# Optimization experiments

Hardware: AMD Instinct MI355X
Metric: run time of the kernel (lower is better)

The kernel has to match this reference:

```python
import jax, jax.numpy as jnp
import numpy as np

B, S = 2, 1024
ENC_IN, MARK_IN = 21, 4
PRED_LEN, C_OUT = 96, 21
E = 512                 # embedding_dim
INNER = 2 * E           # proj_factor=2.0 (library default; Model does not pass it)
NH = 8                  # mLSTM heads
DH = INNER // NH        # 128
K = 4                   # causal conv1d kernel
BS = 4                  # qkv_proj_blocksize
NHP = INNER // BS       # 256 block-diagonal proj heads
NB = 4                  # num_blocks
EPS = 1e-5


def setup_inputs() -> dict:
    key = jax.random.key(0)
    ks = jax.random.split(key, 24)
    it = iter(range(24))
    def n(shape, s=0.02):
        return jax.random.normal(ks[next(it)], shape, jnp.float32) * s
    return {
        "x_enc": n((B, S, ENC_IN), 1.0),
        "x_mark_enc": n((B, S, MARK_IN), 1.0),
        "x_dec": n((B, PRED_LEN, ENC_IN), 1.0),
        "x_mark_dec": n((B, PRED_LEN, MARK_IN), 1.0),
        "emb_W": n((ENC_IN + MARK_IN, E), 0.05),
        "emb_b": jnp.zeros((E,), jnp.float32),
        "ln_w": jnp.ones((NB, E), jnp.float32),
        "up_W": n((NB, E, 2 * INNER)),
        "conv_W": n((NB, INNER, K), 0.1),
        "conv_b": jnp.zeros((NB, INNER), jnp.float32),
        "q_W": n((NB, NHP, BS, BS), 0.1),
        "k_W": n((NB, NHP, BS, BS), 0.1),
        "v_W": n((NB, NHP, BS, BS), 0.1),
        "ig_W": n((NB, 3 * INNER, NH)),
        "ig_b": jnp.zeros((NB, NH), jnp.float32),
        "fg_W": n((NB, 3 * INNER, NH)),
        "fg_b": jnp.tile(jnp.linspace(3.0, 6.0, NH, dtype=jnp.float32), (NB, 1)),
        "skip": jnp.ones((NB, INNER), jnp.float32),
        "onorm_w": jnp.ones((NB, INNER), jnp.float32),
        "down_W": n((NB, INNER, E)),
        "post_ln_w": jnp.ones((E,), jnp.float32),
        "head_W": n((E, C_OUT), 0.05),
        "head_b": jnp.zeros((C_OUT,), jnp.float32),
    }


def _ln(x, w):
    mu = jnp.mean(x, -1, keepdims=True)
    var = jnp.var(x, -1, keepdims=True)
    return (x - mu) * jax.lax.rsqrt(var + EPS) * w


def _headwise(x, w):
    # block-diagonal LinearHeadwiseExpand: (B,S,INNER) with (NHP,BS,BS) blocks
    xh = x.reshape(x.shape[0], x.shape[1], NHP, BS)
    return jnp.einsum('bshd,hod->bsho', xh, w).reshape(x.shape)


def _block(x, lw, uW, cW, cb, qW, kW, vW, igW, igb, fgW, fgb, sk, ow, dW):
    xn = _ln(x, lw)
    up = xn @ uW                                  # (B,S,2*INNER)
    xm, z = up[..., :INNER], up[..., INNER:]
    # causal depthwise conv1d + SiLU
    xc = jax.lax.conv_general_dilated(
        xm.transpose(0, 2, 1), cW[:, None, :], (1,), [(K - 1, 0)],
        feature_group_count=INNER,
        dimension_numbers=('NCH', 'OIH', 'NCH')).transpose(0, 2, 1) + cb
    xc = jax.nn.silu(xc)
    q = _headwise(xc, qW)
    k = _headwise(xc, kW)
    v = _headwise(xm, vW)
    qkv = jnp.concatenate([q, k, v], -1)          # (B,S,3*INNER)
    ig = (qkv @ igW + igb).transpose(0, 2, 1)     # (B,NH,S)
    fg = (qkv @ fgW + fgb).transpose(0, 2, 1)
    qh = q.reshape(B, S, NH, DH).transpose(0, 2, 1, 3)
    kh = k.reshape(B, S, NH, DH).transpose(0, 2, 1, 3)
    vh = v.reshape(B, S, NH, DH).transpose(0, 2, 1, 3)
    # parallel stabilized mLSTM (exp-gated linear attention)
    log_f = jax.nn.log_sigmoid(fg)
    cs = jnp.cumsum(log_f, -1)                    # (B,NH,S)
    Mmat = cs[..., :, None] - cs[..., None, :]    # (B,NH,S,S) cumulative decay
    tri = jnp.tril(jnp.ones((S, S), bool))
    logD = jnp.where(tri, Mmat + ig[..., None, :], -jnp.inf)
    m = jnp.max(logD, -1, keepdims=True)          # row-wise stabilizer
    D = jnp.exp(logD - m)
    qk = jnp.einsum('bnsd,bntd->bnst', qh, kh) / (DH ** 0.5)
    C = qk * D
    norm = jnp.maximum(jnp.abs(jnp.sum(C, -1, keepdims=True)), jnp.exp(-m))
    h = jnp.einsum('bnst,bntd->bnsd', C / (norm + 1e-6), vh)
    # multi-head layernorm (groupnorm over DH per head), weight, no bias
    hn = (h - jnp.mean(h, -1, keepdims=True)) * jax.lax.rsqrt(jnp.var(h, -1, keepdims=True) + EPS)
    hn = hn.transpose(0, 2, 1, 3).reshape(B, S, INNER) * ow
    hs = (hn + sk * xc) * jax.nn.silu(z)          # learnable skip + output gate
    return x + hs @ dW                            # residual


def reference(x_enc, x_mark_enc, x_dec, x_mark_dec, emb_W, emb_b, ln_w, up_W,
              conv_W, conv_b, q_W, k_W, v_W, ig_W, ig_b, fg_W, fg_b, skip,
              onorm_w, down_W, post_ln_w, head_W, head_b):
    x = jnp.concatenate([x_enc, x_mark_enc], -1) @ emb_W + emb_b
    for i in range(NB):
        x = _block(x, ln_w[i], up_W[i], conv_W[i], conv_b[i], q_W[i], k_W[i],
                   v_W[i], ig_W[i], ig_b[i], fg_W[i], fg_b[i], skip[i],
                   onorm_w[i], down_W[i])
    x = _ln(x, post_ln_w)
    return x[:, -PRED_LEN:, :] @ head_W + head_b
```

## Files before the change

kernel.cpp:

```cpp
#include <hip/hip_runtime.h>
#include <hip/hip_bf16.h>

#define S_LEN 1024
#define E_DIM 512
#define INNER_D 1024
#define NHEAD 8
#define DHEAD 128

typedef unsigned short u16;
typedef unsigned int u32;
typedef __attribute__((ext_vector_type(8))) short short8;
typedef __attribute__((ext_vector_type(4))) float f32x4;

union S8 { short8 v; u16 u[8]; uint4 q; };

__device__ __forceinline__ u16 f2bf(float f) {
  u32 u = __float_as_uint(f);
  u32 r = u + 0x7FFFu + ((u >> 16) & 1u);
  return (u16)(r >> 16);
}
__device__ __forceinline__ float bf2f(u16 u) { return __uint_as_float(((u32)u) << 16); }

__device__ __forceinline__ void gload16(const u16* g, u16* l) {
  __builtin_amdgcn_global_load_lds((const __attribute__((address_space(1))) void*)g,
                                   (__attribute__((address_space(3))) void*)l, 16, 0, 0);
}

__device__ __forceinline__ void prep_transpose(
    const float* __restrict__ in, u16* __restrict__ out, int K, int N,
    int k0, int n0, int t, u16 (*T)[72])
{
  int kr = t >> 2, nseg = (t & 3) * 16;
  const float* src = in + (size_t)(k0 + kr) * N + n0 + nseg;
#pragma unroll
  for (int j = 0; j < 16; j++) T[kr][nseg + j] = f2bf(src[j]);
  __syncthreads();
  int nr = t >> 2, kseg = (t & 3) * 16;
  u32 u[8];
#pragma unroll
  for (int rr = 0; rr < 8; rr++) {
    u32 lo = T[kseg + 2 * rr][nr];
    u32 hi = T[kseg + 2 * rr + 1][nr];
    u[rr] = lo | (hi << 16);
  }
  u16* dst = out + (size_t)(n0 + nr) * K + k0 + kseg;
  uint4 w0 = {u[0], u[1], u[2], u[3]};
  uint4 w1 = {u[4], u[5], u[6], u[7]};
  *(uint4*)dst = w0;
  *(uint4*)(dst + 8) = w1;
}

__global__ __launch_bounds__(256) void prep_kernel(
    const float* __restrict__ up_W, u16* __restrict__ upWt,
    const float* __restrict__ down_W, u16* __restrict__ dnWt,
    const float* __restrict__ igW, const float* __restrict__ fgW,
    u16* __restrict__ ghi, u16* __restrict__ glo,
    const float* __restrict__ xe, const float* __restrict__ xmk,
    const float* __restrict__ eW, const float* __restrict__ eb,
    float* __restrict__ x)
{
  __shared__ u16 T[64][72];
  __shared__ float in_s[25];
  int id = blockIdx.x;
  int t = threadIdx.x;
  if (id < 1024) {
    int bx = id & 7, rest = id >> 3;
    int by = rest & 31, L = rest >> 5;
    prep_transpose(up_W + (size_t)L * 512 * 2048, upWt + (size_t)L * 1048576,
                   512, 2048, bx * 64, by * 64, t, T);
  } else if (id < 1536) {
    int id2 = id - 1024;
    int bx = id2 & 15, rest = id2 >> 4;
    int by = rest & 7, L = rest >> 3;
    prep_transpose(down_W + (size_t)L * 1024 * 512, dnWt + (size_t)L * 524288,
                   1024, 512, bx * 64, by * 64, t, T);
  } else if (id < 2304) {
    int id3 = id - 1536;
    int bx = id3 % 12, rest = id3 / 12;
    int n = rest & 15, L = rest >> 4;
    int k = bx * 256 + t;
    const float* W = ((n < 8) ? igW : fgW) + (size_t)L * 24576;
    float v = W[(size_t)k * 8 + (n & 7)];
    u16 h = f2bf(v);
    u16 l = f2bf(v - bf2f(h));
    size_t o = ((size_t)L * 16 + n) * 3072 + k;
    ghi[o] = h;
    glo[o] = l;
  } else {
    int row = id - 2304;
    if (t < 21) in_s[t] = xe[row * 21 + t];
    else if (t < 25) in_s[t] = xmk[row * 4 + t - 21];
    __syncthreads();
#pragma unroll
    for (int rep = 0; rep < 2; rep++) {
      int e = t + rep * 256;
      float acc = eb[e];
#pragma unroll
      for (int i = 0; i < 25; i++) acc += in_s[i] * eW[i * E_DIM + e];
      x[(size_t)row * E_DIM + e] = acc;
    }
  }
}

__global__ __launch_bounds__(256) void ln_kernel(
    const float* __restrict__ x, const float* __restrict__ w, u16* __restrict__ out)
{
  int row = blockIdx.x, tid = threadIdx.x;
  const float* xr = x + (size_t)row * E_DIM;
  float2 v = *(const float2*)(xr + tid * 2);
  float s = v.x + v.y, q = v.x * v.x + v.y * v.y;
#pragma unroll
  for (int off = 32; off; off >>= 1) { s += __shfl_xor(s, off); q += __shfl_xor(q, off); }
  __shared__ float ssum[4], ssq[4];
  int wv = tid >> 6;
  if ((tid & 63) == 0) { ssum[wv] = s; ssq[wv] = q; }
  __syncthreads();
  s = ssum[0] + ssum[1] + ssum[2] + ssum[3];
  q = ssq[0] + ssq[1] + ssq[2] + ssq[3];
  float mu = s * (1.f / E_DIM);
  float var = q * (1.f / E_DIM) - mu * mu;
  float rs = rsqrtf(var + 1e-5f);
  int e = tid * 2;
  ushort2 o;
  o.x = f2bf((v.x - mu) * rs * w[e]);
  o.y = f2bf((v.y - mu) * rs * w[e + 1]);
  *(ushort2*)(out + (size_t)row * E_DIM + e) = o;
}

__global__ __launch_bounds__(256) void lnhead_kernel(
    const float* __restrict__ x, const float* __restrict__ w,
    const float* __restrict__ hW, const float* __restrict__ hb,
    float* __restrict__ out)
{
  int ridx = blockIdx.x;
  int b = ridx / 96, r = ridx % 96;
  int row = b * S_LEN + (S_LEN - 96) + r;
  int tid = threadIdx.x;
  const float* xr = x + (size_t)row * E_DIM;
  float2 v = *(const float2*)(xr + tid * 2);
  float s = v.x + v.y, q = v.x * v.x + v.y * v.y;
#pragma unroll
  for (int off = 32; off; off >>= 1) { s += __shfl_xor(s, off); q += __shfl_xor(q, off); }
  __shared__ float ssum[4], ssq[4];
  __shared__ float lnv[512];
  __shared__ float part[8][32];
  int wv = tid >> 6;
  if ((tid & 63) == 0) { ssum[wv] = s; ssq[wv] = q; }
  __syncthreads();
  s = ssum[0] + ssum[1] + ssum[2] + ssum[3];
  q = ssq[0] + ssq[1] + ssq[2] + ssq[3];
  float mu = s * (1.f / E_DIM);
  float var = q * (1.f / E_DIM) - mu * mu;
  float rs = rsqrtf(var + 1e-5f);
  int e = tid * 2;
  lnv[e]     = (v.x - mu) * rs * w[e];
  lnv[e + 1] = (v.y - mu) * rs * w[e + 1];
  __syncthreads();
  int n = tid & 31, sl = tid >> 5;
  float p = 0.f;
  if (n < 21) {
#pragma unroll 8
    for (int kk = 0; kk < 64; kk++)
      p += lnv[sl * 64 + kk] * hW[(sl * 64 + kk) * 21 + n];
  }
  part[sl][n] = p;
  __syncthreads();
  if (tid < 21) {
    float acc = hb[tid];
#pragma unroll
    for (int j = 0; j < 8; j++) acc += part[j][tid];
    out[ridx * 21 + tid] = acc;
  }
}

__global__ __launch_bounds__(256) void gemm_bf16_split64(
    const u16* __restrict__ A, const u16* __restrict__ Bt,
    float* __restrict__ C0, u16* __restrict__ C1,
    int M, int N, int K, int split_col, int ldc)
{
  __shared__ u16 As0[128 * 32], As1[128 * 32], As2[128 * 32];
  __shared__ u16 Bs0[128 * 32], Bs1[128 * 32], Bs2[128 * 32];
  const int tid = threadIdx.x;
  const int row0 = blockIdx.y * 128, col0 = blockIdx.x * 128;
  const int wave = tid >> 6, lane = tid & 63;
  const int wr = wave >> 1, wc = wave & 1;
  const int lm = lane & 15, lq = lane >> 4;
  const int lr4 = lane >> 2;
  const int cg4 = (lane & 3) ^ (lr4 & 3);
  f32x4 acc[4][4] = {};
  const u16* Abase = A + (size_t)(row0 + lr4) * K + cg4 * 8;
  const u16* Bbase = Bt + (size_t)(col0 + lr4) * K + cg4 * 8;
  const int key = lm & 3;

#define STG_UP(AS, BS, K0) do { \
  _Pragma("unroll") for (int i = 0; i < 2; i++) \
    gload16(Abase + (size_t)((wave * 2 + i) * 16) * K + (K0), &AS[(wave * 2 + i) * 512]); \
  _Pragma("unroll") for (int i = 0; i < 2; i++) \
    gload16(Bbase + (size_t)((wave * 2 + i) * 16) * K + (K0), &BS[(wave * 2 + i) * 512]); \
} while (0)

#define CMP_UP(AS, BS) do { \
  short8 af[4], bfv[4]; \
  _Pragma("unroll") for (int i = 0; i < 4; i++) \
    af[i] = *(const short8*)&AS[(wr * 64 + i * 16 + lm) * 32 + ((lq ^ key) * 8)]; \
  _Pragma("unroll") for (int j = 0; j < 4; j++) \
    bfv[j] = *(const short8*)&BS[(wc * 64 + j * 16 + lm) * 32 + ((lq ^ key) * 8)]; \
  _Pragma("unroll") for (int i = 0; i < 4; i++) \
    _Pragma("unroll") for (int j = 0; j < 4; j++) \
      acc[i][j] = __builtin_amdgcn_mfma_f32_16x16x32_bf16(af[i], bfv[j], acc[i][j], 0, 0, 0); \
} while (0)

  STG_UP(As0, Bs0, 0);
  asm volatile("" ::: "memory");
  STG_UP(As1, Bs1, 32);
  asm volatile("" ::: "memory");
  STG_UP(As2, Bs2, 64);
#pragma unroll
  for (int t = 0; t < 16; t++) {
    if (t <= 13)      asm volatile("s_waitcnt vmcnt(8)" ::: "memory");
    else if (t == 14) asm volatile("s_waitcnt vmcnt(4)" ::: "memory");
    else              asm volatile("s_waitcnt vmcnt(0)" ::: "memory");
    __builtin_amdgcn_sched_barrier(0);
    __builtin_amdgcn_s_barrier();
    if ((t % 3) == 0)      CMP_UP(As0, Bs0);
    else if ((t % 3) == 1) CMP_UP(As1, Bs1);
    else                   CMP_UP(As2, Bs2);
    __builtin_amdgcn_s_barrier();
    if (t + 3 < 16) {
      if ((t % 3) == 0)      STG_UP(As0, Bs0, (t + 3) * 32);
      else if ((t % 3) == 1) STG_UP(As1, Bs1, (t + 3) * 32);
      else                   STG_UP(As2, Bs2, (t + 3) * 32);
    }
  }
#undef STG_UP
#undef CMP_UP

  const bool toC1 = (col0 >= split_col);
#pragma unroll
  for (int i = 0; i < 4; i++) {
#pragma unroll
    for (int j = 0; j < 4; j++) {
      int col = col0 - (toC1 ? split_col : 0) + wc * 64 + j * 16 + lm;
#pragma unroll
      for (int r = 0; r < 4; r++) {
        int row = row0 + wr * 64 + i * 16 + lq * 4 + r;
        if (toC1) C1[(size_t)row * ldc + col] = f2bf(acc[i][j][r]);
        else C0[(size_t)row * ldc + col] = acc[i][j][r];
      }
    }
  }
}

__global__ __launch_bounds__(256) void gemm_bf16_32(
    const u16* __restrict__ A, const u16* __restrict__ Bt,
    float* __restrict__ C, int M, int N, int K, int ldc)
{
  __shared__ u16 As0[64 * 64], As1[64 * 64], As2[64 * 64];
  __shared__ u16 Bs0[64 * 64], Bs1[64 * 64], Bs2[64 * 64];
  const int tid = threadIdx.x;
  const int row0 = blockIdx.y * 64, col0 = blockIdx.x * 64;
  const int wave = tid >> 6, lane = tid & 63;
  const int wr = wave >> 1, wc = wave & 1;
  const int lm = lane & 15, lq = lane >> 4;
  const int lr = lane >> 3;
  const int cg = (lane & 7) ^ lr;
  f32x4 acc[2][2] = {};
  const u16* Abase = A + (size_t)(row0 + lr) * K + cg * 8;
  const u16* Bbase = Bt + (size_t)(col0 + lr) * K + cg * 8;
  const int key = lm & 7;

#define STAGE_DN(AS, BS, K0) do { \
  _Pragma("unroll") for (int i = 0; i < 2; i++) \
    gload16(Abase + (size_t)((wave * 2 + i) * 8) * K + (K0), &AS[(wave * 2 + i) * 512]); \
  _Pragma("unroll") for (int j = 0; j < 2; j++) \
    gload16(Bbase + (size_t)((wave * 2 + j) * 8) * K + (K0), &BS[(wave * 2 + j) * 512]); \
} while (0)

#define COMPUTE_DN(AS, BS) do { \
  short8 af[2][2], bfv[2][2]; \
  _Pragma("unroll") for (int kc = 0; kc < 2; kc++) { \
    _Pragma("unroll") for (int i = 0; i < 2; i++) \
      af[kc][i] = *(const short8*)&AS[(wr * 32 + i * 16 + lm) * 64 + (((kc * 4 + lq) ^ key) * 8)]; \
    _Pragma("unroll") for (int j = 0; j < 2; j++) \
      bfv[kc][j] = *(const short8*)&BS[(wc * 32 + j * 16 + lm) * 64 + (((kc * 4 + lq) ^ key) * 8)]; \
  } \
  _Pragma("unroll") for (int kc = 0; kc < 2; kc++) \
    _Pragma("unroll") for (int i = 0; i < 2; i++) \
      _Pragma("unroll") for (int j = 0; j < 2; j++) \
        acc[i][j] = __builtin_amdgcn_mfma_f32_16x16x32_bf16(af[kc][i], bfv[kc][j], acc[i][j], 0, 0, 0); \
} while (0)

  STAGE_DN(As0, Bs0, 0);
  asm volatile("" ::: "memory");
  STAGE_DN(As1, Bs1, 64);
  asm volatile("" ::: "memory");
  STAGE_DN(As2, Bs2, 128);
#pragma unroll
  for (int t = 0; t < 16; t++) {
    if (t <= 13)      asm volatile("s_waitcnt vmcnt(8)" ::: "memory");
    else if (t == 14) asm volatile("s_waitcnt vmcnt(4)" ::: "memory");
    else              asm volatile("s_waitcnt vmcnt(0)" ::: "memory");
    __builtin_amdgcn_sched_barrier(0);
    __builtin_amdgcn_s_barrier();
    if ((t % 3) == 0)      COMPUTE_DN(As0, Bs0);
    else if ((t % 3) == 1) COMPUTE_DN(As1, Bs1);
    else                   COMPUTE_DN(As2, Bs2);
    __builtin_amdgcn_s_barrier();
    if (t + 3 < 16) {
      if ((t % 3) == 0)      STAGE_DN(As0, Bs0, (t + 3) * 64);
      else if ((t % 3) == 1) STAGE_DN(As1, Bs1, (t + 3) * 64);
      else                   STAGE_DN(As2, Bs2, (t + 3) * 64);
    }
  }
#undef STAGE_DN
#undef COMPUTE_DN

#pragma unroll
  for (int i = 0; i < 2; i++) {
#pragma unroll
    for (int j = 0; j < 2; j++) {
      int col = col0 + wc * 32 + j * 16 + lm;
#pragma unroll
      for (int r = 0; r < 4; r++) {
        int row = row0 + wr * 32 + i * 16 + lq * 4 + r;
        C[(size_t)row * ldc + col] += acc[i][j][r];
      }
    }
  }
}

__global__ __launch_bounds__(256) void convqkv_kernel(
    const float* __restrict__ xm,
    const float* __restrict__ cw, const float* __restrict__ cb,
    const float* __restrict__ qw, const float* __restrict__ kw, const float* __restrict__ vw,
    float* __restrict__ xc, u16* __restrict__ q, u16* __restrict__ k, u16* __restrict__ v,
    u16* __restrict__ vt)
{
  int r0 = blockIdx.x * 8;
  int s0 = r0 & (S_LEN - 1);
  int g = threadIdx.x;
  int c0 = g * 4;
  const float* base = xm + (size_t)r0 * INNER_D + c0;

  float4 xv[11];
#pragma unroll
  for (int j = 0; j < 11; j++) {
    int ts = s0 - 3 + j;
    float4 t = {0.f, 0.f, 0.f, 0.f};
    if (ts >= 0) t = *(const float4*)(base + (ptrdiff_t)(j - 3) * INNER_D);
    xv[j] = t;
  }
  float cwv[4][4];
#pragma unroll
  for (int c = 0; c < 4; c++)
#pragma unroll
    for (int kk = 0; kk < 4; kk++) cwv[c][kk] = cw[(c0 + c) * 4 + kk];
  float cbv[4] = {cb[c0], cb[c0 + 1], cb[c0 + 2], cb[c0 + 3]};
  const float* qg = qw + g * 16;
  const float* kg = kw + g * 16;
  const float* vg = vw + g * 16;
  float qwv[16], kwv[16], vwv[16];
#pragma unroll
  for (int i = 0; i < 16; i++) { qwv[i] = qg[i]; kwv[i] = kg[i]; vwv[i] = vg[i]; }

  u32 vt_pack[4][4];

#pragma unroll
  for (int i = 0; i < 8; i++) {
    float a0 = cbv[0], a1 = cbv[1], a2 = cbv[2], a3 = cbv[3];
#pragma unroll
    for (int kk = 0; kk < 4; kk++) {
      float4 xvv = xv[i + kk];
      a0 += xvv.x * cwv[0][kk];
      a1 += xvv.y * cwv[1][kk];
      a2 += xvv.z * cwv[2][kk];
      a3 += xvv.w * cwv[3][kk];
    }
    a0 = a0 / (1.f + __expf(-a0));
    a1 = a1 / (1.f + __expf(-a1));
    a2 = a2 / (1.f + __expf(-a2));
    a3 = a3 / (1.f + __expf(-a3));
    float4 accv = {a0, a1, a2, a3};
    *(float4*)(xc + (size_t)(r0 + i) * INNER_D + c0) = accv;

    float xcv[4] = {a0, a1, a2, a3};
    float xmv[4] = {xv[i + 3].x, xv[i + 3].y, xv[i + 3].z, xv[i + 3].w};
    ushort4 qs, ks, vs;
    u16* qp = (u16*)&qs; u16* kp = (u16*)&ks; u16* vp = (u16*)&vs;
#pragma unroll
    for (int o = 0; o < 4; o++) {
      float aq = 0.f, ak = 0.f, av = 0.f;
#pragma unroll
      for (int d = 0; d < 4; d++) {
        aq += xcv[d] * qwv[o * 4 + d];
        ak += xcv[d] * kwv[o * 4 + d];
        av += xmv[d] * vwv[o * 4 + d];
      }
      qp[o] = f2bf(aq); kp[o] = f2bf(ak);
      u16 vv = f2bf(av);
      vp[o] = vv;
      if ((i & 1) == 0) vt_pack[o][i >> 1] = (u32)vv;
      else              vt_pack[o][i >> 1] |= ((u32)vv) << 16;
    }
    size_t off = (size_t)(r0 + i) * INNER_D + c0;
    *(ushort4*)(q + off) = qs;
    *(ushort4*)(k + off) = ks;
    *(ushort4*)(v + off) = vs;
  }
  u16* vtb = vt + ((size_t)((r0 >> 10) * INNER_D + c0)) * S_LEN + s0;
#pragma unroll
  for (int c = 0; c < 4; c++) {
    uint4 wv4 = {vt_pack[c][0], vt_pack[c][1], vt_pack[c][2], vt_pack[c][3]};
    *(uint4*)(vtb + (size_t)c * S_LEN) = wv4;
  }
}

__global__ __launch_bounds__(256) void gates_mfma_kernel(
    const u16* __restrict__ q, const u16* __restrict__ k, const u16* __restrict__ v,
    const u16* __restrict__ whi, const u16* __restrict__ wlo,
    const float* __restrict__ igb, const float* __restrict__ fgb,
    float* __restrict__ ig, float* __restrict__ fg)
{
  const int blk = blockIdx.x;
  const int tid = threadIdx.x;
  const int wave = tid >> 6, lane = tid & 63;
  const int lm = lane & 15, lq = lane >> 4;
  const int grow = blk * 16 + lm;
  const u16* parts[3] = {q, k, v};
  f32x4 acc = {};
#pragma unroll 4
  for (int kc = 0; kc < 24; kc++) {
    int k0 = wave * 768 + kc * 32;
    int part = k0 >> 10;
    int idx = (k0 & 1023) + lq * 8;
    S8 a, bh_, bl_;
    a.q = *(const uint4*)(parts[part] + (size_t)grow * INNER_D + idx);
    bh_.q = *(const uint4*)(whi + (size_t)lm * 3072 + k0 + lq * 8);
    bl_.q = *(const uint4*)(wlo + (size_t)lm * 3072 + k0 + lq * 8);
    __builtin_amdgcn_s_setprio(1);
    acc = __builtin_amdgcn_mfma_f32_16x16x32_bf16(a.v, bh_.v, acc, 0, 0, 0);
    acc = __builtin_amdgcn_mfma_f32_16x16x32_bf16(a.v, bl_.v, acc, 0, 0, 0);
    __builtin_amdgcn_s_setprio(0);
  }
  __shared__ float red[4][16][17];
#pragma unroll
  for (int r = 0; r < 4; r++) red[wave][lq * 4 + r][lm] = acc[r];
  __syncthreads();
  if (wave == 0) {
#pragma unroll
    for (int r = 0; r < 4; r++) {
      int row = lq * 4 + r;
      float sum = red[0][row][lm] + red[1][row][lm] + red[2][row][lm] + red[3][row][lm];
      int growr = blk * 16 + row;
      int b = growr >> 10, s = growr & (S_LEN - 1);
      if (lm < 8) ig[((size_t)(b * NHEAD + lm) << 10) + s] = sum + igb[lm];
      else        fg[((size_t)(b * NHEAD + (lm - 8)) << 10) + s] = sum + fgb[lm - 8];
    }
  }
}

__global__ __launch_bounds__(1024) void scan_kernel(
    const float* __restrict__ ig, const float* __restrict__ fg,
    float* __restrict__ a, float* __restrict__ rm, float* __restrict__ enm)
{
  int bh = blockIdx.x;
  int t = threadIdx.x;
  int lane = t & 63, wv = t >> 6;
  __shared__ float sw[16];
  size_t o = ((size_t)bh << 10) + t;
  float f = fg[o];
  float lf = (f >= 0.f) ? -log1pf(__expf(-f)) : f - log1pf(__expf(f));
  float v = lf;
#pragma unroll
  for (int off = 1; off < 64; off <<= 1) {
    float u = __shfl_up(v, off);
    if (lane >= off) v += u;
  }
  if (lane == 63) sw[wv] = v;
  __syncthreads();
  float pre = 0.f;
  for (int w = 0; w < wv; w++) pre += sw[w];
  float cs = v + pre;
  float av = ig[o] - cs;
  a[o] = av;
  float m = av;
#pragma unroll
  for (int off = 1; off < 64; off <<= 1) {
    float u = __shfl_up(m, off);
    if (lane >= off) m = fmaxf(m, u);
  }
  __syncthreads();
  if (lane == 63) sw[wv] = m;
  __syncthreads();
  float pm = -3.4e38f;
  for (int w = 0; w < wv; w++) pm = fmaxf(pm, sw[w]);
  float rmx = fmaxf(m, pm);
  rm[o] = rmx;
  enm[o] = __expf(-(cs + rmx));
}

__device__ __constant__ int c_qt[24] = {7,15,14,15, 6,13,14,12,13, 5,11,12,10,11, 4, 9,10, 8, 9, 3, 8, 2, 1, 0};
__device__ __constant__ int c_k0[24] = {0, 0, 7, 8, 0, 0, 0, 6, 7, 0, 0, 0, 5, 6, 0, 0, 0, 4, 5, 0, 0, 0, 0, 0};
__device__ __constant__ int c_k1[24] = {8, 8,15,16, 7, 7, 7,13,14, 6, 6, 6,11,12, 5, 5, 5, 9,10, 4, 4, 3, 2, 1};
__device__ __constant__ int c_md[24] = {0, 1, 2, 2, 0, 1, 1, 2, 2, 0, 1, 1, 2, 2, 0, 1, 1, 2, 2, 0, 1, 0, 0, 0};

__global__ __launch_bounds__(256) void attn_mfma_kernel(
    const u16* __restrict__ qhg, const u16* __restrict__ khg, const u16* __restrict__ vtg,
    const float* __restrict__ a_arr, const float* __restrict__ rm_arr, const float* __restrict__ enm_arr,
    const float* __restrict__ xc, const u16* __restrict__ zh,
    const float* __restrict__ skip, const float* __restrict__ onw,
    u16* __restrict__ hs, float* __restrict__ hpart, float* __restrict__ scpart)
{
  const int bh = blockIdx.x;
  const int job = blockIdx.y;
  const int qt = c_qt[job], k0t = c_k0[job], k1t = c_k1[job], mode = c_md[job];
  const int b = bh >> 3, h = bh & 7;
  const int s0 = qt * 64;
  const int tid = threadIdx.x;
  const int wave = tid >> 6, lane = tid & 63;
  const int lm = lane & 15, lq = lane >> 4;
  const size_t rowbase = (size_t)b * S_LEN;
  const int c0 = h * DHEAD;

  __shared__ u16 Ks0[64 * 128], Ks1[64 * 128];
  __shared__ u16 Vt0[128 * 64], Vt1[128 * 64];
  __shared__ u16 Ws[64 * 72];

  short8 aq[4];
  {
    const u16* qp = qhg + (rowbase + s0 + wave * 16 + lm) * INNER_D + c0 + lq * 8;
#pragma unroll
    for (int kc = 0; kc < 4; kc++) {
      S8 tmp; tmp.q = *(const uint4*)(qp + kc * 32);
      aq[kc] = tmp.v;
    }
  }
  const float scale = 0.08838834764831845f;
  float rmv[4], er[4];
#pragma unroll
  for (int r = 0; r < 4; r++) {
    rmv[r] = rm_arr[(size_t)bh * S_LEN + s0 + wave * 16 + lq * 4 + r];
    er[r] = scale * __expf(-rmv[r]);
  }

  f32x4 accH[8] = {};
  float sc_acc[4] = {0.f, 0.f, 0.f, 0.f};
  const int lr16 = lane >> 4;
  const int ls16 = lane & 15;
  const int lr8 = lane >> 3;
  const int cgv = (lane & 7) ^ lr8;
  const u16* vtbase = vtg + ((size_t)b * INNER_D + c0) * S_LEN;

  float ae0[4], ae1[4];

#define PREF(KS, VS, AE, T0) do { \
  _Pragma("unroll") for (int j = 0; j < 4; j++) { \
    int rK = (wave * 4 + j) * 4 + lr16; \
    int cgk = ls16 ^ (rK & 7); \
    gload16(khg + (rowbase + (T0) + rK) * INNER_D + c0 + cgk * 8, &KS[(wave * 4 + j) * 512]); \
  } \
  _Pragma("unroll") for (int j = 0; j < 4; j++) { \
    int rV = (wave * 4 + j) * 8 + lr8; \
    gload16(vtbase + (size_t)rV * S_LEN + (T0) + cgv * 8, &VS[(wave * 4 + j) * 512]); \
  } \
  _Pragma("unroll") for (int cb = 0; cb < 4; cb++) \
    AE[cb] = a_arr[(size_t)bh * S_LEN + (T0) + cb * 16 + lm]; \
} while (0)

#define QK_STEP(KS, PACC) do { \
  __builtin_amdgcn_s_setprio(1); \
  _Pragma("unroll") for (int kc = 0; kc < 4; kc++) \
    _Pragma("unroll") for (int cb = 0; cb < 4; cb++) { \
      short8 bk = *(const short8*)&KS[(cb * 16 + lm) * 128 + (((kc * 4 + lq) ^ (lm & 7)) * 8)]; \
      PACC[cb] = __builtin_amdgcn_mfma_f32_16x16x32_bf16(aq[kc], bk, PACC[cb], 0, 0, 0); \
    } \
  __builtin_amdgcn_s_setprio(0); \
} while (0)

#define W_PV(AE, VT, T0, PACC) do { \
  float wpart[4] = {0.f, 0.f, 0.f, 0.f}; \
  _Pragma("unroll") for (int cb = 0; cb < 4; cb++) { \
    int colg = (T0) + cb * 16 + lm; \
    float ec = __expf(AE[cb]); \
    _Pragma("unroll") for (int r = 0; r < 4; r++) { \
      int rowg = s0 + wave * 16 + lq * 4 + r; \
      float wv = PACC[cb][r] * ec * er[r]; \
      if (colg > rowg) wv = 0.f; \
      wpart[r] += wv; \
      Ws[(wave * 16 + lq * 4 + r) * 72 + cb * 16 + lm] = f2bf(wv); \
    } \
  } \
  _Pragma("unroll") for (int r = 0; r < 4; r++) { \
    float sr = wpart[r]; \
    sr += __shfl_xor(sr, 1); sr += __shfl_xor(sr, 2); \
    sr += __shfl_xor(sr, 4); sr += __shfl_xor(sr, 8); \
    sc_acc[r] += sr; \
  } \
  __builtin_amdgcn_s_setprio(1); \
  _Pragma("unroll") for (int kc = 0; kc < 2; kc++) { \
    short8 aw = *(const short8*)&Ws[(wave * 16 + lm) * 72 + kc * 32 + lq * 8]; \
    _Pragma("unroll") for (int nb = 0; nb < 8; nb++) { \
      short8 bv = *(const short8*)&VT[(nb * 16 + lm) * 64 + (((kc * 4 + lq) ^ (lm & 7)) * 8)]; \
      accH[nb] = __builtin_amdgcn_mfma_f32_16x16x32_bf16(aw, bv, accH[nb], 0, 0, 0); \
    } \
  } \
  __builtin_amdgcn_s_setprio(0); \
} while (0)

  int kt = k0t;
  PREF(Ks0, Vt0, ae0, kt * 64);
  asm volatile("" ::: "memory");
  if (kt + 1 < k1t) PREF(Ks1, Vt1, ae1, (kt + 1) * 64);

  while (true) {
    {
      if (kt + 1 < k1t) asm volatile("s_waitcnt vmcnt(12)" ::: "memory");
      else              asm volatile("s_waitcnt vmcnt(0)" ::: "memory");
      __builtin_amdgcn_sched_barrier(0);
      __builtin_amdgcn_s_barrier();
      f32x4 pacc[4] = {};
      QK_STEP(Ks0, pacc);
      W_PV(ae0, Vt0, kt * 64, pacc);
      __builtin_amdgcn_s_barrier();
      if (kt + 2 < k1t) PREF(Ks0, Vt0, ae0, (kt + 2) * 64);
      kt++;
      if (kt >= k1t) break;
    }
    {
      if (kt + 1 < k1t) asm volatile("s_waitcnt vmcnt(12)" ::: "memory");
      else              asm volatile("s_waitcnt vmcnt(0)" ::: "memory");
      __builtin_amdgcn_sched_barrier(0);
      __builtin_amdgcn_s_barrier();
      f32x4 pacc[4] = {};
      QK_STEP(Ks1, pacc);
      W_PV(ae1, Vt1, kt * 64, pacc);
      __builtin_amdgcn_s_barrier();
      if (kt + 2 < k1t) PREF(Ks1, Vt1, ae1, (kt + 2) * 64);
      kt++;
      if (kt >= k1t) break;
    }
  }
#undef PREF
#undef QK_STEP
#undef W_PV

  if (mode != 0) {
    int slot = mode - 1;
    int qr = qt - 8;
    float* Hp = hpart + (((size_t)slot * 16 + bh) * 8 + qr) * 8192;
    float* sp = scpart + ((slot * 16 + bh) * 8 + qr) * 64;
#pragma unroll
    for (int r = 0; r < 4; r++) {
      int row = wave * 16 + lq * 4 + r;
      if (lm == 0) sp[row] = sc_acc[r];
#pragma unroll
      for (int nb = 0; nb < 8; nb++)
        Hp[row * 128 + nb * 16 + lm] = accH[nb][r];
    }
    return;
  }

  float inv[4], muv[4], rsv[4];
#pragma unroll
  for (int r = 0; r < 4; r++) {
    int rowg = s0 + wave * 16 + lq * 4 + r;
    float nrm = fmaxf(fabsf(sc_acc[r]), enm_arr[(size_t)bh * S_LEN + rowg]);
    inv[r] = 1.f / (nrm + 1e-6f);
  }
#pragma unroll
  for (int r = 0; r < 4; r++) {
    float s = 0.f, qq = 0.f;
#pragma unroll
    for (int nb = 0; nb < 8; nb++) {
      float hv = accH[nb][r] * inv[r];
      accH[nb][r] = hv;
      s += hv; qq += hv * hv;
    }
    s += __shfl_xor(s, 1); s += __shfl_xor(s, 2); s += __shfl_xor(s, 4); s += __shfl_xor(s, 8);
    qq += __shfl_xor(qq, 1); qq += __shfl_xor(qq, 2); qq += __shfl_xor(qq, 4); qq += __shfl_xor(qq, 8);
    float mu = s * (1.f / DHEAD);
    float var = qq * (1.f / DHEAD) - mu * mu;
    muv[r] = mu;
    rsv[r] = rsqrtf(var + 1e-5f);
  }
  float ow[8], sk[8];
#pragma unroll
  for (int nb = 0; nb < 8; nb++) {
    ow[nb] = onw[c0 + nb * 16 + lm];
    sk[nb] = skip[c0 + nb * 16 + lm];
  }
#pragma unroll
  for (int r = 0; r < 4; r++) {
    int rowg = s0 + wave * 16 + lq * 4 + r;
    size_t base = (rowbase + rowg) * INNER_D + c0;
#pragma unroll
    for (int nb = 0; nb < 8; nb++) {
      int d = nb * 16 + lm;
      float xcv = xc[base + d];
      float zv = bf2f(zh[base + d]);
      float hn = (accH[nb][r] - muv[r]) * rsv[r] * ow[nb] + sk[nb] * xcv;
      float o = hn * (zv / (1.f + __expf(-zv)));
      hs[base + d] = f2bf(o);
    }
  }
}

__global__ __launch_bounds__(256) void attn_combine_kernel(
    const float* __restrict__ hpart, const float* __restrict__ scpart,
    const float* __restrict__ enm,
    const float* __restrict__ xc, const u16* __restrict__ zh,
    const float* __restrict__ skip, const float* __restrict__ onw,
    u16* __restrict__ hs)
{
  int wave = threadIdx.x >> 6, lane = threadIdx.x & 63;
  int gid = blockIdx.x * 4 + wave;
  int bh = gid >> 9;
  int rr = gid & 511;
  int qr = rr >> 6, row = rr & 63;
  int b = bh >> 3, hh = bh & 7;
  int s = (qr + 8) * 64 + row;
  size_t off = (((size_t)bh) * 8 + qr) * 8192 + row * 128 + lane * 2;
  float2 h0 = *(const float2*)(hpart + off);
  float2 h1 = *(const float2*)(hpart + 1048576 + off);
  int sidx = (bh * 8 + qr) * 64 + row;
  float sc = scpart[sidx] + scpart[8192 + sidx];
  float nrm = fmaxf(fabsf(sc), enm[(size_t)bh * S_LEN + s]);
  float inv = 1.f / (nrm + 1e-6f);
  float hx = (h0.x + h1.x) * inv, hy = (h0.y + h1.y) * inv;
  float sm = hx + hy, sq = hx * hx + hy * hy;
#pragma unroll
  for (int off2 = 32; off2; off2 >>= 1) { sm += __shfl_xor(sm, off2); sq += __shfl_xor(sq, off2); }
  float mu = sm * (1.f / DHEAD);
  float var = sq * (1.f / DHEAD) - mu * mu;
  float rs = rsqrtf(var + 1e-5f);
  int c0 = hh * DHEAD + lane * 2;
  size_t base = ((size_t)(b * S_LEN + s)) * INNER_D + c0;
  float2 xc2 = *(const float2*)(xc + base);
  ushort2 z2u = *(const ushort2*)(zh + base);
  float z2x = bf2f(z2u.x), z2y = bf2f(z2u.y);
  float skx = skip[c0], sky = skip[c0 + 1];
  float owx = onw[c0],  owy = onw[c0 + 1];
  ushort2 o;
  o.x = f2bf(((hx - mu) * rs * owx + skx * xc2.x) * (z2x / (1.f + __expf(-z2x))));
  o.y = f2bf(((hy - mu) * rs * owy + sky * xc2.y) * (z2y / (1.f + __expf(-z2y))));
  *(ushort2*)(hs + base) = o;
}

extern "C" void kernel_launch(void* const* d_in, const int* in_sizes, int n_in,
                              void* d_out, int out_size, void* d_ws, size_t ws_size,
                              hipStream_t stream)
{
  const float* x_enc   = (const float*)d_in[0];
  const float* x_mark  = (const float*)d_in[1];
  const float* emb_W   = (const float*)d_in[4];
  const float* emb_b   = (const float*)d_in[5];
  const float* ln_w    = (const float*)d_in[6];
  const float* up_W    = (const float*)d_in[7];
  const float* conv_W  = (const float*)d_in[8];
  const float* conv_b  = (const float*)d_in[9];
  const float* q_W     = (const float*)d_in[10];
  const float* k_W     = (const float*)d_in[11];
  const float* v_W     = (const float*)d_in[12];
  const float* ig_W    = (const float*)d_in[13];
  const float* ig_b    = (const float*)d_in[14];
  const float* fg_W    = (const float*)d_in[15];
  const float* fg_b    = (const float*)d_in[16];
  const float* skip_w  = (const float*)d_in[17];
  const float* onorm_w = (const float*)d_in[18];
  const float* down_W  = (const float*)d_in[19];
  const float* post_ln = (const float*)d_in[20];
  const float* head_W  = (const float*)d_in[21];
  const float* head_b  = (const float*)d_in[22];

  float* p = (float*)d_ws;
  float* x    = p; p += 1048576;
  float* xm   = p; p += 2097152;
  float* xc   = p; p += 2097152;
  float* igb_ = p; p += 16384;
  float* fgb_ = p; p += 16384;
  float* ab   = p; p += 16384;
  float* rmb  = p; p += 16384;
  float* enmb = p; p += 16384;
  u16* qhb = (u16*)p; p += 1048576;
  u16* khb = (u16*)p; p += 1048576;
  u16* vhb = (u16*)p; p += 1048576;
  u16* zh  = (u16*)p; p += 524288;
  u16* xnh = (u16*)p; p += 524288;
  u16* upWtA = (u16*)p; p += 2097152;
  u16* dnWtA = (u16*)p; p += 1048576;
  u16* gtwH = (u16*)p; p += 98304;
  u16* gtwL = (u16*)p; p += 98304;
  float* hpart = p; p += 2097152;
  float* scpart = p; p += 16384;
  u16* vtg = (u16*)p; p += 1048576;
  u16* hsbh = (u16*)xm;

  prep_kernel<<<4352, 256, 0, stream>>>(
      up_W, upWtA, down_W, dnWtA, ig_W, fg_W, gtwH, gtwL,
      x_enc, x_mark, emb_W, emb_b, x);

  for (int L = 0; L < 4; L++) {
    ln_kernel<<<2048, 256, 0, stream>>>(x, ln_w + L * 512, xnh);
    gemm_bf16_split64<<<dim3(16, 16), 256, 0, stream>>>(
        xnh, upWtA + (size_t)L * 1048576, xm, zh, 2048, 2048, 512, 1024, 1024);
    convqkv_kernel<<<256, 256, 0, stream>>>(
        xm, conv_W + L * 4096, conv_b + L * 1024,
        q_W + L * 4096, k_W + L * 4096, v_W + L * 4096,
        xc, qhb, khb, vhb, vtg);
    gates_mfma_kernel<<<128, 256, 0, stream>>>(
        qhb, khb, vhb, gtwH + (size_t)L * 49152, gtwL + (size_t)L * 49152,
        ig_b + L * 8, fg_b + L * 8, igb_, fgb_);
    scan_kernel<<<16, 1024, 0, stream>>>(igb_, fgb_, ab, rmb, enmb);
    attn_mfma_kernel<<<dim3(16, 24), 256, 0, stream>>>(
        qhb, khb, vtg, ab, rmb, enmb, xc, zh,
        skip_w + L * 1024, onorm_w + L * 1024, hsbh, hpart, scpart);
    attn_combine_kernel<<<2048, 256, 0, stream>>>(
        hpart, scpart, enmb, xc, zh, skip_w + L * 1024, onorm_w + L * 1024, hsbh);
    gemm_bf16_32<<<dim3(8, 32), 256, 0, stream>>>(
        hsbh, dnWtA + (size_t)L * 524288, x, 2048, 512, 1024, 512);
  }

  lnhead_kernel<<<192, 256, 0, stream>>>(x, post_ln, head_W, head_b, (float*)d_out);
}
```

Before: 447.7 us.

## Split causal attention KV range into finer chunks across more blocks

The causal mLSTM attention work split is reorganized from 24 jobs per head (up to 8 KV tiles each, at most 2 partial slots) into 40 jobs with at most about 4 KV tiles each. Query tiles 4-15 now write up to 4 partial H/score slots that the combine kernel sums before normalization. The aim is better load balance and more blocks in flight on the many-CU GPU. The cost is larger partial buffers, more global traffic for the partials, and a heavier combine pass.

```diff
diff --git a/kernel.cpp b/kernel.cpp
--- a/kernel.cpp
+++ b/kernel.cpp
@@ -499,10 +499,21 @@
   enm[o] = __expf(-(cs + rmx));
 }
 
-__device__ __constant__ int c_qt[24] = {7,15,14,15, 6,13,14,12,13, 5,11,12,10,11, 4, 9,10, 8, 9, 3, 8, 2, 1, 0};
-__device__ __constant__ int c_k0[24] = {0, 0, 7, 8, 0, 0, 0, 6, 7, 0, 0, 0, 5, 6, 0, 0, 0, 4, 5, 0, 0, 0, 0, 0};
-__device__ __constant__ int c_k1[24] = {8, 8,15,16, 7, 7, 7,13,14, 6, 6, 6,11,12, 5, 5, 5, 9,10, 4, 4, 3, 2, 1};
-__device__ __constant__ int c_md[24] = {0, 1, 2, 2, 0, 1, 1, 2, 2, 0, 1, 1, 2, 2, 0, 1, 1, 2, 2, 0, 1, 0, 0, 0};
+__device__ __constant__ int c_qt[40] = {15,15,15,15, 14,14,14,14, 13,13,13,13, 12,12,12,12,
+                                        11,11,11, 10,10,10, 9,9,9, 8,8,8,
+                                        7,7, 6,6, 5,5, 4,4, 3, 2, 1, 0};
+__device__ __constant__ int c_k0[40] = {0,4,8,12, 0,4,8,12, 0,4,8,11, 0,4,7,10,
+                                        0,4,8, 0,4,8, 0,4,7, 0,3,6,
+                                        0,4, 0,4, 0,3, 0,3, 0, 0, 0, 0};
+__device__ __constant__ int c_k1[40] = {4,8,12,16, 4,8,12,15, 4,8,11,14, 4,7,10,13,
+                                        4,8,12, 4,8,11, 4,7,10, 3,6,9,
+                                        4,8, 4,7, 3,6, 3,5, 4, 3, 2, 1};
+__device__ __constant__ int c_md[40] = {1,2,3,4, 1,2,3,4, 1,2,3,4, 1,2,3,4,
+                                        1,2,3, 1,2,3, 1,2,3, 1,2,3,
+                                        1,2, 1,2, 1,2, 1,2, 0, 0, 0, 0};
+
+#define HP_SLOT 1572864
+#define SC_SLOT 12288
 
 __global__ __launch_bounds__(256) void attn_mfma_kernel(
     const u16* __restrict__ qhg, const u16* __restrict__ khg, const u16* __restrict__ vtg,
@@ -646,9 +657,9 @@
 
   if (mode != 0) {
     int slot = mode - 1;
-    int qr = qt - 8;
-    float* Hp = hpart + (((size_t)slot * 16 + bh) * 8 + qr) * 8192;
-    float* sp = scpart + ((slot * 16 + bh) * 8 + qr) * 64;
+    int qr = qt - 4;
+    float* Hp = hpart + (size_t)slot * HP_SLOT + ((size_t)(bh * 12 + qr)) * 8192;
+    float* sp = scpart + slot * SC_SLOT + (bh * 12 + qr) * 64;
 #pragma unroll
     for (int r = 0; r < 4; r++) {
       int row = wave * 16 + lq * 4 + r;
@@ -714,19 +725,23 @@
 {
   int wave = threadIdx.x >> 6, lane = threadIdx.x & 63;
   int gid = blockIdx.x * 4 + wave;
-  int bh = gid >> 9;
-  int rr = gid & 511;
+  int bh = gid / 768;
+  int rr = gid % 768;
   int qr = rr >> 6, row = rr & 63;
   int b = bh >> 3, hh = bh & 7;
-  int s = (qr + 8) * 64 + row;
-  size_t off = (((size_t)bh) * 8 + qr) * 8192 + row * 128 + lane * 2;
-  float2 h0 = *(const float2*)(hpart + off);
-  float2 h1 = *(const float2*)(hpart + 1048576 + off);
-  int sidx = (bh * 8 + qr) * 64 + row;
-  float sc = scpart[sidx] + scpart[8192 + sidx];
+  int s = (qr + 4) * 64 + row;
+  int nsl = 2 + (qr >> 2);
+  size_t off = (((size_t)(bh * 12 + qr)) * 64 + row) * 128 + lane * 2;
+  int sidx = (bh * 12 + qr) * 64 + row;
+  float hx = 0.f, hy = 0.f, sc = 0.f;
+  for (int sl = 0; sl < nsl; sl++) {
+    float2 hp = *(const float2*)(hpart + (size_t)sl * HP_SLOT + off);
+    hx += hp.x; hy += hp.y;
+    sc += scpart[sl * SC_SLOT + sidx];
+  }
   float nrm = fmaxf(fabsf(sc), enm[(size_t)bh * S_LEN + s]);
   float inv = 1.f / (nrm + 1e-6f);
-  float hx = (h0.x + h1.x) * inv, hy = (h0.y + h1.y) * inv;
+  hx *= inv; hy *= inv;
   float sm = hx + hy, sq = hx * hx + hy * hy;
 #pragma unroll
   for (int off2 = 32; off2; off2 >>= 1) { sm += __shfl_xor(sm, off2); sq += __shfl_xor(sq, off2); }
@@ -784,14 +799,14 @@
   u16* qhb = (u16*)p; p += 1048576;
   u16* khb = (u16*)p; p += 1048576;
   u16* vhb = (u16*)p; p += 1048576;
-  u16* zh  = (u16*)p; p += 524288;
+  u16* zh  = (u16*)p; p += 1048576;
   u16* xnh = (u16*)p; p += 524288;
   u16* upWtA = (u16*)p; p += 2097152;
   u16* dnWtA = (u16*)p; p += 1048576;
   u16* gtwH = (u16*)p; p += 98304;
   u16* gtwL = (u16*)p; p += 98304;
-  float* hpart = p; p += 2097152;
-  float* scpart = p; p += 16384;
+  float* hpart = p; p += 6291456;
+  float* scpart = p; p += 49152;
   u16* vtg = (u16*)p; p += 1048576;
   u16* hsbh = (u16*)xm;
 
@@ -811,10 +826,10 @@
         qhb, khb, vhb, gtwH + (size_t)L * 49152, gtwL + (size_t)L * 49152,
         ig_b + L * 8, fg_b + L * 8, igb_, fgb_);
     scan_kernel<<<16, 1024, 0, stream>>>(igb_, fgb_, ab, rmb, enmb);
-    attn_mfma_kernel<<<dim3(16, 24), 256, 0, stream>>>(
+    attn_mfma_kernel<<<dim3(16, 40), 256, 0, stream>>>(
         qhb, khb, vtg, ab, rmb, enmb, xc, zh,
         skip_w + L * 1024, onorm_w + L * 1024, hsbh, hpart, scpart);
-    attn_combine_kernel<<<2048, 256, 0, stream>>>(
+    attn_combine_kernel<<<3072, 256, 0, stream>>>(
         hpart, scpart, enmb, xc, zh, skip_w + L * 1024, onorm_w + L * 1024, hsbh);
     gemm_bf16_32<<<dim3(8, 32), 256, 0, stream>>>(
         hsbh, dnWtA + (size_t)L * 524288, x, 2048, 512, 1024, 512);
```

Result: slower. 460.5 us (+2.9%).
